# Kernel optimization log

Hardware: AMD Instinct MI355X
Metric: run time of the kernel (lower is better)

## Reference

```python
import jax, jax.numpy as jnp
import numpy as np

E, TOPK, D, F, FS = 16, 4, 2560, 1664, 3328
B, S = 1, 2048


def setup_inputs() -> dict:
    key = jax.random.key(0)
    ks = jax.random.split(key, 8)
    sc = lambda *sh: 1.0 / np.sqrt(sh[-2] if len(sh) > 1 else 1.0)
    return {
        "hidden_states": jax.random.normal(ks[0], (B, S, D), jnp.float32),
        "router_weight": jax.random.normal(ks[1], (E, D), jnp.float32) * (1.0 / np.sqrt(D)),
        "w_gate": jax.random.normal(ks[2], (E, D, F), jnp.float32) * (1.0 / np.sqrt(D)),
        "w_up": jax.random.normal(ks[3], (E, D, F), jnp.float32) * (1.0 / np.sqrt(D)),
        "w_down": jax.random.normal(ks[4], (E, F, D), jnp.float32) * (1.0 / np.sqrt(F)),
        "sw_gate": jax.random.normal(ks[5], (D, FS), jnp.float32) * (1.0 / np.sqrt(D)),
        "sw_up": jax.random.normal(ks[6], (D, FS), jnp.float32) * (1.0 / np.sqrt(D)),
        "sw_down": jax.random.normal(ks[7], (FS, D), jnp.float32) * (1.0 / np.sqrt(FS)),
    }


def reference(hidden_states, router_weight, w_gate, w_up, w_down, sw_gate, sw_up, sw_down):
    b, s, d = hidden_states.shape
    x = hidden_states.reshape(-1, d)  # [T, D]
    T = x.shape[0]

    # Router: linear -> softmax -> top-k -> renormalize (vLLM FusedMoE default)
    logits = x @ router_weight.T                      # [T, E]
    probs = jax.nn.softmax(logits, axis=-1)
    topk_w, topk_idx = jax.lax.top_k(probs, TOPK)     # [T, K]
    topk_w = topk_w / jnp.sum(topk_w, axis=-1, keepdims=True)
    combine = jnp.zeros((T, E), x.dtype).at[jnp.arange(T)[:, None], topk_idx].add(topk_w)  # [T, E]

    # Expert SiLU-gated MLPs (dense-dispatch reference for grouped GEMM)
    g = jnp.einsum('td,edf->tef', x, w_gate)          # [T, E, F]
    u = jnp.einsum('td,edf->tef', x, w_up)
    h = jax.nn.silu(g) * u
    y = jnp.einsum('tef,efd->ted', h, w_down)         # [T, E, D]
    sparse_out = jnp.einsum('ted,te->td', y, combine)

    # Shared expert: LlamaMLP with silu gate, no bias
    shared_out = (jax.nn.silu(x @ sw_gate) * (x @ sw_up)) @ sw_down

    return (sparse_out + shared_out).reshape(b, s, d)
```

## Files before the change

### kernel.cpp

```cpp
#include <hip/hip_runtime.h>
#include <hip/hip_bf16.h>
#include <stdint.h>

#define E_N 16
#define TOPK 4
#define DD 2560
#define FF 1664
#define FSS 3328
#define TT 2048

#define BK 32

typedef __attribute__((ext_vector_type(8))) __bf16 bf16x8;
typedef __attribute__((ext_vector_type(4))) float f32x4;

__device__ __forceinline__ unsigned short f2bf(float f) {
  return __builtin_bit_cast(unsigned short, (__bf16)f);
}
__device__ __forceinline__ float bf2f(unsigned short u) {
  return __builtin_bit_cast(float, (unsigned int)u << 16);
}
__device__ __forceinline__ unsigned int pk2(float a, float b) {
  return (unsigned int)f2bf(a) | ((unsigned int)f2bf(b) << 16);
}

#define GLOAD16(g, l)                                                          \
  __builtin_amdgcn_global_load_lds(                                            \
      (const __attribute__((address_space(1))) void*)(g),                      \
      (__attribute__((address_space(3))) void*)(l), 16, 0, 0)

#define SBAR() __builtin_amdgcn_s_barrier()
#define SCHED0() __builtin_amdgcn_sched_barrier(0)
#define VMW(N) asm volatile("s_waitcnt vmcnt(" #N ")" ::: "memory")

__device__ __forceinline__ void swz_block(int& bm, int& bn, int& bz) {
  int gx = gridDim.x, gy = gridDim.y;
  int nwg = gx * gy * gridDim.z;
  int flat = blockIdx.x + gx * (blockIdx.y + gy * blockIdx.z);
  if ((nwg & 7) == 0) flat = (flat & 7) * (nwg >> 3) + (flat >> 3);
  bm = flat % gx;
  int rest = flat / gx;
  bn = rest % gy;
  bz = rest / gy;
}

__global__ __launch_bounds__(256) void cvt_bf16_kernel(const float* __restrict__ in,
                                                       unsigned short* __restrict__ out) {
  size_t i = ((size_t)blockIdx.x * 256 + threadIdx.x) * 4;
  float4 v = *reinterpret_cast<const float4*>(in + i);
  ushort4 o;
  o.x = f2bf(v.x); o.y = f2bf(v.y); o.z = f2bf(v.z); o.w = f2bf(v.w);
  *reinterpret_cast<ushort4*>(out + i) = o;
}

__global__ __launch_bounds__(256) void tcvt_kernel(const float* __restrict__ in,
                                                   unsigned short* __restrict__ out,
                                                   int K, int N) {
  __shared__ float lds[64 * 65];
  int z = blockIdx.z;
  in += (size_t)z * K * N;
  out += (size_t)z * K * N;
  int k0 = blockIdx.x * 64, n0 = blockIdx.y * 64;
  int t = threadIdx.x;
#pragma unroll
  for (int j = 0; j < 4; ++j) {
    int idx = j * 256 + t;
    int r = idx >> 4, c = (idx & 15) * 4;
    float4 v = *reinterpret_cast<const float4*>(in + (size_t)(k0 + r) * N + n0 + c);
    lds[r * 65 + c] = v.x;
    lds[r * 65 + c + 1] = v.y;
    lds[r * 65 + c + 2] = v.z;
    lds[r * 65 + c + 3] = v.w;
  }
  __syncthreads();
#pragma unroll
  for (int j = 0; j < 2; ++j) {
    int idx = j * 256 + t;
    int n = idx >> 3, kg = (idx & 7) * 8;
    float a0 = lds[(kg + 0) * 65 + n], a1 = lds[(kg + 1) * 65 + n];
    float a2 = lds[(kg + 2) * 65 + n], a3 = lds[(kg + 3) * 65 + n];
    float a4 = lds[(kg + 4) * 65 + n], a5 = lds[(kg + 5) * 65 + n];
    float a6 = lds[(kg + 6) * 65 + n], a7 = lds[(kg + 7) * 65 + n];
    uint4 o{pk2(a0, a1), pk2(a2, a3), pk2(a4, a5), pk2(a6, a7)};
    *reinterpret_cast<uint4*>(out + (size_t)(n0 + n) * K + k0 + kg) = o;
  }
}

__global__ __launch_bounds__(256) void router_kernel(const float* __restrict__ x,
                                                     const float* __restrict__ rw,
                                                     int* __restrict__ cnt,
                                                     int* __restrict__ list,
                                                     float* __restrict__ tw) {
  int t = blockIdx.x;
  const float* xr = x + (size_t)t * DD;
  __shared__ float logits[E_N];
  int lane = threadIdx.x & 63, wid = threadIdx.x >> 6;
  for (int ee = 0; ee < 4; ++ee) {
    int e = wid * 4 + ee;
    const float* wr = rw + (size_t)e * DD;
    float p = 0.f;
    for (int d = lane; d < DD; d += 64) p += xr[d] * wr[d];
#pragma unroll
    for (int off = 32; off > 0; off >>= 1) p += __shfl_down(p, off);
    if (lane == 0) logits[e] = p;
  }
  __syncthreads();
  if (threadIdx.x == 0) {
    float mx = -1e30f;
    for (int e = 0; e < E_N; ++e) mx = fmaxf(mx, logits[e]);
    float pe[E_N];
    for (int e = 0; e < E_N; ++e) pe[e] = __expf(logits[e] - mx);
    int idx[TOPK]; float val[TOPK]; float s4 = 0.f;
    unsigned used = 0;
    for (int k = 0; k < TOPK; ++k) {
      int bi = 0; float bv = -1.f;
      for (int e = 0; e < E_N; ++e)
        if (!((used >> e) & 1) && pe[e] > bv) { bv = pe[e]; bi = e; }
      used |= 1u << bi; idx[k] = bi; val[k] = bv; s4 += bv;
    }
    float inv = 1.f / s4;
    for (int k = 0; k < TOPK; ++k) {
      int e2 = idx[k];
      int pos = atomicAdd(&cnt[e2], 1);
      list[e2 * TT + pos] = t * 4 + k;
      tw[t * 4 + k] = val[k] * inv;
    }
  }
}

template <int MODE>
__global__ __launch_bounds__(512, 2) void g1_kernel(
    const unsigned short* __restrict__ Ab,
    const unsigned short* __restrict__ WT,
    void* __restrict__ Out,
    const int* __restrict__ list, const int* __restrict__ cnt,
    const float* __restrict__ tw,
    int Ktot, int Ntot, int Mfixed) {
  int bm, bn, e;
  swz_block(bm, bn, e);
  int M = cnt ? cnt[e] : Mfixed;
  int m0 = bm * 256;
  if (m0 >= M) return;
  int n0 = bn * 256;
  const unsigned short* B0 = WT + (size_t)e * Ktot * Ntot;
  const int* lst = list ? (list + e * TT) : nullptr;

  __shared__ __align__(16) unsigned short lds[4][16384];

  int tid = threadIdx.x, lane = tid & 63, w = tid >> 6;
  int wm = w >> 2, wn = w & 3;

  const unsigned short* pA[2];
  const unsigned short* pB[2];
#pragma unroll
  for (int j = 0; j < 2; ++j) {
    int idx = j * 512 + tid;
    int row = idx >> 2, c = idx & 3;
    int cs = c ^ ((row >> 1) & 3);
    int ar = min(m0 + row, M - 1);
    int code = lst ? lst[ar] : ar;
    int arow = (MODE == 0) ? (lst ? (code >> 2) : code) : code;
    pA[j] = Ab + (size_t)arow * Ktot + cs * 8;
    int br = min(n0 + row, Ntot - 1);
    pB[j] = B0 + (size_t)br * Ktot + cs * 8;
  }

  auto issue = [&](int kt, int buf) {
    int koff = kt * BK;
    unsigned short* d = &lds[buf][0];
#pragma unroll
    for (int j = 0; j < 2; ++j)
      GLOAD16(pA[j] + koff, d + (j * 512 + tid) * 8);
#pragma unroll
    for (int j = 0; j < 2; ++j)
      GLOAD16(pB[j] + koff, d + 8192 + (j * 512 + tid) * 8);
  };

  int cg = lane >> 4;
  int aoff[8], boff[4];
#pragma unroll
  for (int mf = 0; mf < 8; ++mf) {
    int r = wm * 128 + mf * 16 + (lane & 15);
    aoff[mf] = r * 32 + ((cg ^ ((r >> 1) & 3)) * 8);
  }
#pragma unroll
  for (int nf = 0; nf < 4; ++nf) {
    int rb = wn * 64 + nf * 16 + (lane & 15);
    boff[nf] = 8192 + rb * 32 + ((cg ^ ((rb >> 1) & 3)) * 8);
  }

  f32x4 acc[8][4] = {};

  auto compute = [&](int buf) {
    const unsigned short* L = &lds[buf][0];
    bf16x8 a[8], b[4];
#pragma unroll
    for (int mf = 0; mf < 8; ++mf)
      a[mf] = __builtin_bit_cast(bf16x8, *reinterpret_cast<const uint4*>(L + aoff[mf]));
#pragma unroll
    for (int nf = 0; nf < 4; ++nf)
      b[nf] = __builtin_bit_cast(bf16x8, *reinterpret_cast<const uint4*>(L + boff[nf]));
    __builtin_amdgcn_s_setprio(1);
#pragma unroll
    for (int mf = 0; mf < 8; ++mf)
#pragma unroll
      for (int nf = 0; nf < 4; ++nf)
        acc[mf][nf] = __builtin_amdgcn_mfma_f32_16x16x32_bf16(a[mf], b[nf], acc[mf][nf], 0, 0, 0);
    __builtin_amdgcn_s_setprio(0);
  };

  int nk = Ktot / BK;
  issue(0, 0);
  issue(1, 1);
  issue(2, 2);
  for (int kt = 0; kt < nk; ++kt) {
    int rem = nk - 1 - kt;
    if (rem >= 2) { VMW(8); }
    else if (rem == 1) { VMW(4); }
    else { VMW(0); }
    SCHED0();
    SBAR(); SCHED0();
    if (rem >= 3) { issue(kt + 3, (kt + 3) & 3); SCHED0(); }
    compute(kt & 3);
    SCHED0();
  }

#pragma unroll
  for (int mf = 0; mf < 8; ++mf) {
#pragma unroll
    for (int q = 0; q < 4; ++q) {
      int lr = wm * 128 + mf * 16 + (lane >> 4) * 4 + q;
      int grow = m0 + lr;
      if (grow < M) {
        int code = lst ? lst[grow] : grow;
        int colb = n0 + wn * 64 + (lane & 15);
        if (MODE == 0) {
          unsigned short* Op = (unsigned short*)Out + (size_t)code * Ntot + colb;
#pragma unroll
          for (int nf = 0; nf < 4; ++nf)
            if (colb + nf * 16 < Ntot) Op[nf * 16] = f2bf(acc[mf][nf][q]);
        } else {
          float scale = tw ? tw[code] : 1.f;
          float* Op = (float*)Out + (size_t)code * Ntot + colb;
#pragma unroll
          for (int nf = 0; nf < 4; ++nf)
            if (colb + nf * 16 < Ntot) Op[nf * 16] = acc[mf][nf][q] * scale;
        }
      }
    }
  }
}

__global__ __launch_bounds__(256) void h_kernel(const unsigned short* __restrict__ g,
                                                unsigned short* __restrict__ u) {
  size_t i = ((size_t)blockIdx.x * 256 + threadIdx.x) * 8;
  uint4 gv = *reinterpret_cast<const uint4*>(g + i);
  uint4 uv = *reinterpret_cast<const uint4*>(u + i);
  const unsigned int* gw = reinterpret_cast<const unsigned int*>(&gv);
  const unsigned int* uw = reinterpret_cast<const unsigned int*>(&uv);
  uint4 ov;
  unsigned int* ow = reinterpret_cast<unsigned int*>(&ov);
#pragma unroll
  for (int j = 0; j < 4; ++j) {
    float g0 = bf2f((unsigned short)(gw[j] & 0xffff));
    float g1 = bf2f((unsigned short)(gw[j] >> 16));
    float u0 = bf2f((unsigned short)(uw[j] & 0xffff));
    float u1 = bf2f((unsigned short)(uw[j] >> 16));
    float h0 = (g0 / (1.f + __expf(-g0))) * u0;
    float h1 = (g1 / (1.f + __expf(-g1))) * u1;
    ow[j] = pk2(h0, h1);
  }
  *reinterpret_cast<uint4*>(u + i) = ov;
}

__global__ __launch_bounds__(256) void combine_kernel(const float* __restrict__ Y,
                                                      const float* __restrict__ Ys,
                                                      float* __restrict__ out) {
  size_t i = ((size_t)blockIdx.x * 256 + threadIdx.x) * 4;
  size_t t = i / DD;
  int d = (int)(i % DD);
  float4 a = *reinterpret_cast<const float4*>(Ys + i);
#pragma unroll
  for (int k = 0; k < 4; ++k) {
    float4 v = *reinterpret_cast<const float4*>(Y + (t * 4 + k) * (size_t)DD + d);
    a.x += v.x; a.y += v.y; a.z += v.z; a.w += v.w;
  }
  *reinterpret_cast<float4*>(out + i) = a;
}

extern "C" void kernel_launch(void* const* d_in, const int* in_sizes, int n_in,
                              void* d_out, int out_size, void* d_ws, size_t ws_size,
                              hipStream_t stream) {
  const float* x  = (const float*)d_in[0];
  const float* rw = (const float*)d_in[1];
  const float* wg = (const float*)d_in[2];
  const float* wu = (const float*)d_in[3];
  const float* wd = (const float*)d_in[4];
  const float* sg = (const float*)d_in[5];
  const float* su = (const float*)d_in[6];
  const float* sd = (const float*)d_in[7];
  float* out = (float*)d_out;

  char* ws = (char*)d_ws;
  size_t off = 0;
  auto alloc = [&](size_t bytes) {
    off = (off + 255) & ~(size_t)255;
    void* p = ws + off;
    off += bytes;
    return p;
  };
  unsigned short* W1 = (unsigned short*)alloc((size_t)E_N * FF * DD * 2);
  unsigned short* W2 = (unsigned short*)alloc((size_t)E_N * FF * DD * 2);
  unsigned short* W3 = (unsigned short*)alloc((size_t)FSS * DD * 2);
  unsigned short* W4 = (unsigned short*)alloc((size_t)FSS * DD * 2);
  unsigned short* Xb = (unsigned short*)alloc((size_t)TT * DD * 2);
  unsigned short* Gx = (unsigned short*)alloc((size_t)4 * TT * FF * 2);
  unsigned short* Hx = (unsigned short*)alloc((size_t)4 * TT * FF * 2);
  unsigned short* Gs = (unsigned short*)alloc((size_t)TT * FSS * 2);
  unsigned short* Hs = (unsigned short*)alloc((size_t)TT * FSS * 2);
  float* Y  = (float*)alloc((size_t)4 * TT * DD * 4);
  float* Ys = (float*)alloc((size_t)TT * DD * 4);
  float* tw = (float*)alloc((size_t)4 * TT * 4);
  int* cnt  = (int*)alloc(E_N * 4);
  int* list = (int*)alloc((size_t)E_N * TT * 4);
  (void)ws_size; (void)in_sizes; (void)n_in; (void)out_size;

  hipMemsetAsync(cnt, 0, E_N * 4, stream);
  cvt_bf16_kernel<<<TT * DD / 4 / 256, 256, 0, stream>>>(x, Xb);
  router_kernel<<<TT, 256, 0, stream>>>(x, rw, cnt, list, tw);

  tcvt_kernel<<<dim3(DD / 64, FF / 64, E_N), 256, 0, stream>>>(wg, W1, DD, FF);
  tcvt_kernel<<<dim3(DD / 64, FF / 64, E_N), 256, 0, stream>>>(wu, W2, DD, FF);
  tcvt_kernel<<<dim3(DD / 64, FSS / 64, 1), 256, 0, stream>>>(sg, W3, DD, FSS);
  tcvt_kernel<<<dim3(DD / 64, FSS / 64, 1), 256, 0, stream>>>(su, W4, DD, FSS);

  g1_kernel<0><<<dim3(TT * 4 / 256, (FF + 255) / 256, E_N), 512, 0, stream>>>(
      Xb, W1, Gx, list, cnt, nullptr, DD, FF, 0);
  g1_kernel<0><<<dim3(TT * 4 / 256, (FF + 255) / 256, E_N), 512, 0, stream>>>(
      Xb, W2, Hx, list, cnt, nullptr, DD, FF, 0);
  h_kernel<<<(size_t)4 * TT * FF / 8 / 256, 256, 0, stream>>>(Gx, Hx);

  g1_kernel<0><<<dim3(TT / 256, FSS / 256, 1), 512, 0, stream>>>(
      Xb, W3, Gs, nullptr, nullptr, nullptr, DD, FSS, TT);
  g1_kernel<0><<<dim3(TT / 256, FSS / 256, 1), 512, 0, stream>>>(
      Xb, W4, Hs, nullptr, nullptr, nullptr, DD, FSS, TT);
  h_kernel<<<(size_t)TT * FSS / 8 / 256, 256, 0, stream>>>(Gs, Hs);

  tcvt_kernel<<<dim3(FF / 64, DD / 64, E_N), 256, 0, stream>>>(wd, W1, FF, DD);
  tcvt_kernel<<<dim3(FSS / 64, DD / 64, 1), 256, 0, stream>>>(sd, W2, FSS, DD);

  g1_kernel<1><<<dim3(TT * 4 / 256, DD / 256, E_N), 512, 0, stream>>>(
      Hx, W1, Y, list, cnt, tw, FF, DD, 0);
  g1_kernel<1><<<dim3(TT / 256, DD / 256, 1), 512, 0, stream>>>(
      Hs, W2, Ys, nullptr, nullptr, nullptr, FSS, DD, TT);

  combine_kernel<<<TT * DD / 4 / 256, 256, 0, stream>>>(Y, Ys, out);
}
```

Before: 1.268 ms.

## Fuse grouped and shared expert GEMMs into single launches with 128x128 tiles

Replaces the 256x256 four-stage pipelined GEMM with a 128x128-tile, single-buffered GEMM body (BK=64, 8-way XOR swizzle). Merges the gate/up expert and shared GEMMs into one launch and the two down GEMMs into another, using the z-dimension to select the expert or shared path. The intent is fewer launches and better load balance over uneven expert counts through more, smaller blocks. In exchange it loses the deep async prefetch pipeline and exposes global-load latency behind a barrier each K step.

```diff
diff --git a/kernel.cpp b/kernel.cpp
--- a/kernel.cpp
+++ b/kernel.cpp
@@ -9,8 +9,6 @@
 #define FSS 3328
 #define TT 2048
 
-#define BK 32
-
 typedef __attribute__((ext_vector_type(8))) __bf16 bf16x8;
 typedef __attribute__((ext_vector_type(4))) float f32x4;
 
@@ -28,10 +26,6 @@
   __builtin_amdgcn_global_load_lds(                                            \
       (const __attribute__((address_space(1))) void*)(g),                      \
       (__attribute__((address_space(3))) void*)(l), 16, 0, 0)
-
-#define SBAR() __builtin_amdgcn_s_barrier()
-#define SCHED0() __builtin_amdgcn_sched_barrier(0)
-#define VMW(N) asm volatile("s_waitcnt vmcnt(" #N ")" ::: "memory")
 
 __device__ __forceinline__ void swz_block(int& bm, int& bn, int& bz) {
   int gx = gridDim.x, gy = gridDim.y;
@@ -128,127 +122,167 @@
   }
 }
 
-template <int MODE>
-__global__ __launch_bounds__(512, 2) void g1_kernel(
-    const unsigned short* __restrict__ Ab,
-    const unsigned short* __restrict__ WT,
-    void* __restrict__ Out,
-    const int* __restrict__ list, const int* __restrict__ cnt,
-    const float* __restrict__ tw,
-    int Ktot, int Ntot, int Mfixed) {
-  int bm, bn, e;
-  swz_block(bm, bn, e);
-  int M = cnt ? cnt[e] : Mfixed;
-  int m0 = bm * 256;
-  if (m0 >= M) return;
-  int n0 = bn * 256;
-  const unsigned short* B0 = WT + (size_t)e * Ktot * Ntot;
-  const int* lst = list ? (list + e * TT) : nullptr;
-
-  __shared__ __align__(16) unsigned short lds[4][16384];
+template <int MODE, int SHIFT>
+__device__ __forceinline__ void gemm_body(
+    const unsigned short* __restrict__ A0, const unsigned short* __restrict__ W0,
+    void* __restrict__ O0, const int* lst, const float* __restrict__ tw,
+    int M, int Kt, int Nt, int m0, int n0) {
+  __shared__ __align__(16) unsigned short ldsA[8192];
+  __shared__ __align__(16) unsigned short ldsB[8192];
 
   int tid = threadIdx.x, lane = tid & 63, w = tid >> 6;
-  int wm = w >> 2, wn = w & 3;
-
-  const unsigned short* pA[2];
-  const unsigned short* pB[2];
-#pragma unroll
-  for (int j = 0; j < 2; ++j) {
-    int idx = j * 512 + tid;
-    int row = idx >> 2, c = idx & 3;
-    int cs = c ^ ((row >> 1) & 3);
+
+  const unsigned short* pA[4];
+  const unsigned short* pB[4];
+#pragma unroll
+  for (int j = 0; j < 4; ++j) {
+    int row = j * 32 + (tid >> 3);
+    int cs = (tid & 7) ^ (row & 7);
     int ar = min(m0 + row, M - 1);
     int code = lst ? lst[ar] : ar;
-    int arow = (MODE == 0) ? (lst ? (code >> 2) : code) : code;
-    pA[j] = Ab + (size_t)arow * Ktot + cs * 8;
-    int br = min(n0 + row, Ntot - 1);
-    pB[j] = B0 + (size_t)br * Ktot + cs * 8;
-  }
-
-  auto issue = [&](int kt, int buf) {
-    int koff = kt * BK;
-    unsigned short* d = &lds[buf][0];
-#pragma unroll
-    for (int j = 0; j < 2; ++j)
-      GLOAD16(pA[j] + koff, d + (j * 512 + tid) * 8);
-#pragma unroll
-    for (int j = 0; j < 2; ++j)
-      GLOAD16(pB[j] + koff, d + 8192 + (j * 512 + tid) * 8);
+    int arow = SHIFT ? (lst ? (code >> 2) : code) : code;
+    pA[j] = A0 + (size_t)arow * Kt + cs * 8;
+    pB[j] = W0 + (size_t)(n0 + j * 32 + (tid >> 3)) * Kt + cs * 8;
+  }
+
+  auto issue = [&](int kt) {
+    int koff = kt * 64;
+#pragma unroll
+    for (int j = 0; j < 4; ++j) {
+      GLOAD16(pA[j] + koff, ldsA + j * 2048 + tid * 8);
+      GLOAD16(pB[j] + koff, ldsB + j * 2048 + tid * 8);
+    }
   };
 
-  int cg = lane >> 4;
-  int aoff[8], boff[4];
-#pragma unroll
-  for (int mf = 0; mf < 8; ++mf) {
-    int r = wm * 128 + mf * 16 + (lane & 15);
-    aoff[mf] = r * 32 + ((cg ^ ((r >> 1) & 3)) * 8);
-  }
-#pragma unroll
-  for (int nf = 0; nf < 4; ++nf) {
-    int rb = wn * 64 + nf * 16 + (lane & 15);
-    boff[nf] = 8192 + rb * 32 + ((cg ^ ((rb >> 1) & 3)) * 8);
-  }
-
-  f32x4 acc[8][4] = {};
-
-  auto compute = [&](int buf) {
-    const unsigned short* L = &lds[buf][0];
-    bf16x8 a[8], b[4];
-#pragma unroll
-    for (int mf = 0; mf < 8; ++mf)
-      a[mf] = __builtin_bit_cast(bf16x8, *reinterpret_cast<const uint4*>(L + aoff[mf]));
-#pragma unroll
-    for (int nf = 0; nf < 4; ++nf)
-      b[nf] = __builtin_bit_cast(bf16x8, *reinterpret_cast<const uint4*>(L + boff[nf]));
-    __builtin_amdgcn_s_setprio(1);
-#pragma unroll
-    for (int mf = 0; mf < 8; ++mf)
-#pragma unroll
-      for (int nf = 0; nf < 4; ++nf)
-        acc[mf][nf] = __builtin_amdgcn_mfma_f32_16x16x32_bf16(a[mf], b[nf], acc[mf][nf], 0, 0, 0);
-    __builtin_amdgcn_s_setprio(0);
-  };
-
-  int nk = Ktot / BK;
-  issue(0, 0);
-  issue(1, 1);
-  issue(2, 2);
+  int wr = (w >> 1) * 64, wc = (w & 1) * 64;
+  int aoff[4][2], boff[4][2];
+#pragma unroll
+  for (int m = 0; m < 4; ++m) {
+    int r = wr + m * 16 + (lane & 15);
+    int rb = wc + m * 16 + (lane & 15);
+#pragma unroll
+    for (int kh = 0; kh < 2; ++kh) {
+      int cg = kh * 4 + (lane >> 4);
+      aoff[m][kh] = r * 64 + ((cg ^ (r & 7)) * 8);
+      boff[m][kh] = rb * 64 + ((cg ^ (rb & 7)) * 8);
+    }
+  }
+
+  f32x4 acc[4][4] = {};
+
+  int nk = Kt / 64;
+  issue(0);
   for (int kt = 0; kt < nk; ++kt) {
-    int rem = nk - 1 - kt;
-    if (rem >= 2) { VMW(8); }
-    else if (rem == 1) { VMW(4); }
-    else { VMW(0); }
-    SCHED0();
-    SBAR(); SCHED0();
-    if (rem >= 3) { issue(kt + 3, (kt + 3) & 3); SCHED0(); }
-    compute(kt & 3);
-    SCHED0();
-  }
-
-#pragma unroll
-  for (int mf = 0; mf < 8; ++mf) {
+    __syncthreads();
+#pragma unroll
+    for (int kh = 0; kh < 2; ++kh) {
+      bf16x8 a[4], b[4];
+#pragma unroll
+      for (int m = 0; m < 4; ++m)
+        a[m] = __builtin_bit_cast(bf16x8, *reinterpret_cast<const uint4*>(ldsA + aoff[m][kh]));
+#pragma unroll
+      for (int n = 0; n < 4; ++n)
+        b[n] = __builtin_bit_cast(bf16x8, *reinterpret_cast<const uint4*>(ldsB + boff[n][kh]));
+      __builtin_amdgcn_s_setprio(1);
+#pragma unroll
+      for (int m = 0; m < 4; ++m)
+#pragma unroll
+        for (int n = 0; n < 4; ++n)
+          acc[m][n] = __builtin_amdgcn_mfma_f32_16x16x32_bf16(a[m], b[n], acc[m][n], 0, 0, 0);
+      __builtin_amdgcn_s_setprio(0);
+    }
+    __syncthreads();
+    if (kt + 1 < nk) issue(kt + 1);
+  }
+
+#pragma unroll
+  for (int m = 0; m < 4; ++m) {
 #pragma unroll
     for (int q = 0; q < 4; ++q) {
-      int lr = wm * 128 + mf * 16 + (lane >> 4) * 4 + q;
+      int lr = wr + m * 16 + (lane >> 4) * 4 + q;
       int grow = m0 + lr;
       if (grow < M) {
         int code = lst ? lst[grow] : grow;
-        int colb = n0 + wn * 64 + (lane & 15);
+        int col = n0 + wc + (lane & 15);
         if (MODE == 0) {
-          unsigned short* Op = (unsigned short*)Out + (size_t)code * Ntot + colb;
-#pragma unroll
-          for (int nf = 0; nf < 4; ++nf)
-            if (colb + nf * 16 < Ntot) Op[nf * 16] = f2bf(acc[mf][nf][q]);
+          unsigned short* Op = (unsigned short*)O0 + (size_t)code * Nt + col;
+#pragma unroll
+          for (int n = 0; n < 4; ++n) Op[n * 16] = f2bf(acc[m][n][q]);
         } else {
           float scale = tw ? tw[code] : 1.f;
-          float* Op = (float*)Out + (size_t)code * Ntot + colb;
-#pragma unroll
-          for (int nf = 0; nf < 4; ++nf)
-            if (colb + nf * 16 < Ntot) Op[nf * 16] = acc[mf][nf][q] * scale;
+          float* Op = (float*)O0 + (size_t)code * Nt + col;
+#pragma unroll
+          for (int n = 0; n < 4; ++n) Op[n * 16] = acc[m][n][q] * scale;
         }
       }
     }
   }
+}
+
+__global__ __launch_bounds__(256, 3) void gu2_kernel(
+    const unsigned short* __restrict__ Xb,
+    const unsigned short* __restrict__ WgT, const unsigned short* __restrict__ WuT,
+    const unsigned short* __restrict__ SgT, const unsigned short* __restrict__ SuT,
+    unsigned short* __restrict__ Gx, unsigned short* __restrict__ Ux,
+    unsigned short* __restrict__ Gs, unsigned short* __restrict__ Us,
+    const int* __restrict__ list, const int* __restrict__ cnt) {
+  int bm, bn, z;
+  swz_block(bm, bn, z);
+  bool up = z >= 17;
+  int ze = up ? z - 17 : z;
+  const unsigned short* W0;
+  unsigned short* O0;
+  const int* lst = nullptr;
+  int M, Nt;
+  if (ze < E_N) {
+    M = cnt[ze];
+    lst = list + ze * TT;
+    Nt = FF;
+    W0 = (up ? WuT : WgT) + (size_t)ze * DD * FF;
+    O0 = up ? Ux : Gx;
+  } else {
+    M = TT;
+    Nt = FSS;
+    W0 = up ? SuT : SgT;
+    O0 = up ? Us : Gs;
+  }
+  int m0 = bm * 128, n0 = bn * 128;
+  if (m0 >= M || n0 >= Nt) return;
+  gemm_body<0, 1>(Xb, W0, O0, lst, nullptr, M, DD, Nt, m0, n0);
+}
+
+__global__ __launch_bounds__(256, 3) void dn2_kernel(
+    const unsigned short* __restrict__ Hx, const unsigned short* __restrict__ Hs,
+    const unsigned short* __restrict__ WdT, const unsigned short* __restrict__ SdT,
+    float* __restrict__ Y, float* __restrict__ Ys,
+    const int* __restrict__ list, const int* __restrict__ cnt,
+    const float* __restrict__ tw) {
+  int bm, bn, z;
+  swz_block(bm, bn, z);
+  const unsigned short* A0;
+  const unsigned short* W0;
+  float* O0;
+  const int* lst = nullptr;
+  const float* sc = nullptr;
+  int M, Kt;
+  if (z < E_N) {
+    M = cnt[z];
+    lst = list + z * TT;
+    Kt = FF;
+    A0 = Hx;
+    W0 = WdT + (size_t)z * FF * DD;
+    O0 = Y;
+    sc = tw;
+  } else {
+    M = TT;
+    Kt = FSS;
+    A0 = Hs;
+    W0 = SdT;
+    O0 = Ys;
+  }
+  int m0 = bm * 128, n0 = bn * 128;
+  if (m0 >= M) return;
+  gemm_body<1, 0>(A0, W0, O0, lst, sc, M, Kt, DD, m0, n0);
 }
 
 __global__ __launch_bounds__(256) void h_kernel(const unsigned short* __restrict__ g,
@@ -334,25 +368,17 @@
   tcvt_kernel<<<dim3(DD / 64, FSS / 64, 1), 256, 0, stream>>>(sg, W3, DD, FSS);
   tcvt_kernel<<<dim3(DD / 64, FSS / 64, 1), 256, 0, stream>>>(su, W4, DD, FSS);
 
-  g1_kernel<0><<<dim3(TT * 4 / 256, (FF + 255) / 256, E_N), 512, 0, stream>>>(
-      Xb, W1, Gx, list, cnt, nullptr, DD, FF, 0);
-  g1_kernel<0><<<dim3(TT * 4 / 256, (FF + 255) / 256, E_N), 512, 0, stream>>>(
-      Xb, W2, Hx, list, cnt, nullptr, DD, FF, 0);
+  gu2_kernel<<<dim3(TT / 128, FSS / 128, 34), 256, 0, stream>>>(
+      Xb, W1, W2, W3, W4, Gx, Hx, Gs, Hs, list, cnt);
+
   h_kernel<<<(size_t)4 * TT * FF / 8 / 256, 256, 0, stream>>>(Gx, Hx);
-
-  g1_kernel<0><<<dim3(TT / 256, FSS / 256, 1), 512, 0, stream>>>(
-      Xb, W3, Gs, nullptr, nullptr, nullptr, DD, FSS, TT);
-  g1_kernel<0><<<dim3(TT / 256, FSS / 256, 1), 512, 0, stream>>>(
-      Xb, W4, Hs, nullptr, nullptr, nullptr, DD, FSS, TT);
   h_kernel<<<(size_t)TT * FSS / 8 / 256, 256, 0, stream>>>(Gs, Hs);
 
   tcvt_kernel<<<dim3(FF / 64, DD / 64, E_N), 256, 0, stream>>>(wd, W1, FF, DD);
   tcvt_kernel<<<dim3(FSS / 64, DD / 64, 1), 256, 0, stream>>>(sd, W2, FSS, DD);
 
-  g1_kernel<1><<<dim3(TT * 4 / 256, DD / 256, E_N), 512, 0, stream>>>(
-      Hx, W1, Y, list, cnt, tw, FF, DD, 0);
-  g1_kernel<1><<<dim3(TT / 256, DD / 256, 1), 512, 0, stream>>>(
-      Hs, W2, Ys, nullptr, nullptr, nullptr, FSS, DD, TT);
+  dn2_kernel<<<dim3(TT / 128, DD / 128, 17), 256, 0, stream>>>(
+      Hx, Hs, W1, W2, Y, Ys, list, cnt, tw);
 
   combine_kernel<<<TT * DD / 4 / 256, 256, 0, stream>>>(Y, Ys, out);
 }
```

Result: faster. 1.195 ms (-5.8%).
